# Performance work log

Measured on AMD Instinct MI355X. Metric: run time of the kernel, lower is better.

Reference implementation:

```python
import jax, jax.numpy as jnp
import numpy as np
from jax import lax

K = 3
PAD = 1
K2 = K * K


def _conv(x, w, b):
    dn = lax.conv_dimension_numbers(x.shape, w.shape, ('NCHW', 'OIHW', 'NCHW'))
    y = lax.conv_general_dilated(x, w, (1, 1), [(PAD, PAD), (PAD, PAD)], dimension_numbers=dn)
    return y + b[None, :, None, None]


def _gather(x, iy, ix):
    # x: [B,C,H,W]; iy,ix: [B,K2,H,W] int32 -> [B,C,K2,H,W]
    B, C, H, W = x.shape
    flat = x.reshape(B, C, H * W)
    idx = iy * W + ix  # [B,K2,H,W]
    return jax.vmap(lambda xb, ib: xb[:, ib])(flat, idx)


def _deform_conv2d(x, offset_w, offset_b, mask_w, mask_b, weight):
    B, C, H, W = x.shape
    O = weight.shape[0]
    offset = _conv(x, offset_w, offset_b)            # [B,2*K2,H,W]
    mask = jax.nn.sigmoid(_conv(x, mask_w, mask_b))  # [B,K2,H,W]

    off = offset.reshape(B, K2, 2, H, W)
    oy, ox = off[:, :, 0], off[:, :, 1]              # [B,K2,H,W]

    ki = (jnp.arange(K2) // K).astype(x.dtype)       # kernel row per tap
    kj = (jnp.arange(K2) % K).astype(x.dtype)        # kernel col per tap
    base_y = (jnp.arange(H) - PAD).astype(x.dtype)
    base_x = (jnp.arange(W) - PAD).astype(x.dtype)

    py = oy + base_y[None, None, :, None] + ki[None, :, None, None]  # [B,K2,H,W]
    px = ox + base_x[None, None, None, :] + kj[None, :, None, None]

    y0 = jnp.floor(py)
    x0 = jnp.floor(px)
    dy = py - y0
    dx = px - x0
    y0i = y0.astype(jnp.int32)
    x0i = x0.astype(jnp.int32)

    acc = jnp.zeros((B, C, K2, H, W), dtype=x.dtype)
    for (yc, xc, wgt) in [
        (y0i,     x0i,     (1 - dy) * (1 - dx)),
        (y0i,     x0i + 1, (1 - dy) * dx),
        (y0i + 1, x0i,     dy * (1 - dx)),
        (y0i + 1, x0i + 1, dy * dx),
    ]:
        valid = ((yc >= 0) & (yc < H) & (xc >= 0) & (xc < W)).astype(x.dtype)
        g = _gather(x, jnp.clip(yc, 0, H - 1), jnp.clip(xc, 0, W - 1))  # [B,C,K2,H,W]
        acc = acc + g * (wgt * valid)[:, None]

    modulated = acc * mask[:, None]                  # [B,C,K2,H,W]
    w2 = weight.reshape(O, C, K2)
    return jnp.einsum('bckhw,ock->bohw', modulated, w2)


def setup_inputs() -> dict:
    key = jax.random.key(0)
    ks = jax.random.split(key, 6)
    B, C, O, H, W = 4, 64, 64, 128, 128
    return {
        'x': jax.random.normal(ks[0], (B, C, H, W), jnp.float32),
        'offset_w': jax.random.normal(ks[1], (2 * K2, C, K, K), jnp.float32) * 0.05,
        'offset_b': jax.random.normal(ks[2], (2 * K2,), jnp.float32) * 0.05,
        'mask_w': jax.random.normal(ks[3], (K2, C, K, K), jnp.float32) * 0.05,
        'mask_b': jnp.full((K2,), 0.5, jnp.float32),
        'weight': jax.random.normal(ks[5], (O, C, K, K), jnp.float32) * (1.0 / np.sqrt(C * K2)),
    }


def reference(x, offset_w, offset_b, mask_w, mask_b, weight):
    return _deform_conv2d(x, offset_w, offset_b, mask_w, mask_b, weight)
```

## Files before the change

### kernel.cpp

```cpp
#include <hip/hip_runtime.h>
#include <math.h>

#define BB 4
#define CC 64
#define OO 64
#define HH 128
#define WW 128
#define HWsz (HH * WW)

typedef __attribute__((ext_vector_type(8))) _Float16 half8;
typedef __attribute__((ext_vector_type(4))) float floatx4;

__global__ __launch_bounds__(256) void pre_kernel(
    const float* __restrict__ x, const float* __restrict__ wgt,
    const float* __restrict__ ow, const float* __restrict__ mw,
    _Float16* __restrict__ xh, _Float16* __restrict__ waf,
    _Float16* __restrict__ wcf)
{
    int bid = blockIdx.x;
    int tid = threadIdx.x;
    if (bid < 512) {
        int b = bid >> 7, y = bid & 127;
        int px = tid & 127;
        int ch = (tid >> 7) * 32;
        const float* xp = x + (size_t)(b * CC + ch) * HWsz + y * WW + px;
        _Float16 buf[32];
#pragma unroll
        for (int q = 0; q < 32; ++q)
            buf[q] = (_Float16)xp[(size_t)q * HWsz];
        _Float16* dst = xh + ((size_t)(b * HH + y) * WW + px) * 64 + ch;
#pragma unroll
        for (int q = 0; q < 4; ++q)
            *(half8*)&dst[q * 8] = *(const half8*)&buf[q * 8];
    } else {
        int i = (bid - 512) * 256 + tid;
        if (i < 36864) {
            int j = i & 7, lane = (i >> 3) & 63, rest = i >> 9;
            int m = rest & 3, kh = (rest >> 2) & 1, k = rest >> 3;
            int o = m * 16 + (lane & 15);
            int c = kh * 32 + ((lane >> 4) << 3) + j;
            waf[i] = (_Float16)wgt[o * 576 + c * 9 + k];
        } else if (i < 55296) {
            int t = i - 36864;
            int j = t & 7, lane = (t >> 3) & 63, rest = t >> 9;
            int m = rest & 1, kh = (rest >> 1) & 1, k = rest >> 2;
            int o = m * 16 + (lane & 15);
            int c = kh * 32 + ((lane >> 4) << 3) + j;
            float v = 0.f;
            if (o < 18) v = ow[o * 576 + c * 9 + k];
            else if (o < 27) v = mw[(o - 18) * 576 + c * 9 + k];
            wcf[t] = (_Float16)v;
        }
    }
}

__global__ __launch_bounds__(1024, 1) void fused_kernel(
    const _Float16* __restrict__ wsrc, const _Float16* __restrict__ xh,
    const float* __restrict__ ob, const float* __restrict__ mb,
    float* __restrict__ out)
{
    __shared__ __align__(16) _Float16 lds_w[55296];
    __shared__ _Float16 omh[16 * 27 * 16];
    __shared__ __align__(16) _Float16 bounce[16 * 1152];

    int tid = threadIdx.x;
    int gid = blockIdx.x;
    int sid = (gid & 7) * 32 + (gid >> 3);
    int b = sid >> 6;
    int t = sid & 63;
    int rq = t >> 1;
    int q = t & 1;

    int wv = tid >> 6;
    int lane = tid & 63;
    int s = wv & 3;
    int h = rq * 4 + (wv >> 2);
    int p0 = q << 6;
    int g = lane >> 4;
    int pl = lane & 15;
    int oct = lane & 7;
    int pxg = lane >> 3;

    const _Float16* xhb = xh + ((size_t)b << 20);
    _Float16* omw = &omh[wv * 27 * 16];
    _Float16* bbw = &bounce[wv * 1152];

#pragma unroll
    for (int it = 0; it < 7; ++it) {
        int c = it * 1024 + tid;
        if (c < 6912)
            *(half8*)&lds_w[c * 8] = *(const half8*)(wsrc + c * 8);
    }
    __syncthreads();

    floatx4 accC0 = {0.f, 0.f, 0.f, 0.f};
    floatx4 accC1 = {0.f, 0.f, 0.f, 0.f};

#define STAGE_ROW(KY) do {                                                   \
    int gy = h + (KY) - 1;                                                   \
    half8 z = {0, 0, 0, 0, 0, 0, 0, 0};                                      \
    _Pragma("unroll") for (int j = 0; j < 3; ++j) {                          \
        int pxi = j * 8 + pxg;                                               \
        bool act = (j < 2) | (pxg < 2);                                      \
        int col = p0 + s * 16 - 1 + pxi;                                     \
        bool val = act & (gy >= 0) & (gy < HH) & (col >= 0) & (col < WW);    \
        half8 v = z;                                                         \
        if (val)                                                             \
            v = *(const half8*)(xhb + (((size_t)gy * WW + col) << 6) + oct * 8); \
        if (act)                                                             \
            *(half8*)&bbw[(pxi << 6) + ((oct ^ (pxi & 7)) << 3)] = v;        \
    }                                                                        \
} while (0)

#define CONVT(KY, KX) do {                                                   \
    int K = (KY) * 3 + (KX);                                                 \
    int pc = pl + (KX);                                                      \
    half8 a0 = *(const half8*)&bbw[(pc << 6) + ((g ^ (pc & 7)) << 3)];       \
    half8 a1 = *(const half8*)&bbw[(pc << 6) + (((g + 4) ^ (pc & 7)) << 3)]; \
    const _Float16* wp = &lds_w[36864 + (K << 11) + lane * 8];               \
    half8 w00 = *(const half8*)(wp + (0 << 9));                              \
    half8 w01 = *(const half8*)(wp + (1 << 9));                              \
    half8 w10 = *(const half8*)(wp + (2 << 9));                              \
    half8 w11 = *(const half8*)(wp + (3 << 9));                              \
    accC0 = __builtin_amdgcn_mfma_f32_16x16x32_f16(w00, a0, accC0, 0, 0, 0); \
    accC1 = __builtin_amdgcn_mfma_f32_16x16x32_f16(w01, a0, accC1, 0, 0, 0); \
    accC0 = __builtin_amdgcn_mfma_f32_16x16x32_f16(w10, a1, accC0, 0, 0, 0); \
    accC1 = __builtin_amdgcn_mfma_f32_16x16x32_f16(w11, a1, accC1, 0, 0, 0); \
} while (0)

    STAGE_ROW(0); CONVT(0, 0); CONVT(0, 1); CONVT(0, 2);
    STAGE_ROW(1); CONVT(1, 0); CONVT(1, 1); CONVT(1, 2);
    STAGE_ROW(2); CONVT(2, 0); CONVT(2, 1); CONVT(2, 2);

#pragma unroll
    for (int j = 0; j < 4; ++j) {
        int o = g * 4 + j;
        omw[o * 16 + pl] = (_Float16)(accC0[j] + ob[o]);
        int o2 = 16 + g * 4 + j;
        float v = accC1[j];
        if (o2 < 18) omw[o2 * 16 + pl] = (_Float16)(v + ob[o2]);
        else if (o2 < 27)
            omw[o2 * 16 + pl] =
                (_Float16)(1.0f / (1.0f + expf(-(v + mb[o2 - 18]))));
    }

    floatx4 acc0 = {0.f, 0.f, 0.f, 0.f}, acc1 = {0.f, 0.f, 0.f, 0.f};
    floatx4 acc2 = {0.f, 0.f, 0.f, 0.f}, acc3 = {0.f, 0.f, 0.f, 0.f};

#define MKT(K, P, U00, U01, U10, U11, I00, I01, I10, I11) do {               \
    int ky = (K) / 3, kx = (K) - ky * 3;                                     \
    float oy = (float)omw[(2 * (K)) * 16 + (P)];                             \
    float ox = (float)omw[(2 * (K) + 1) * 16 + (P)];                         \
    float mk = (float)omw[(18 + (K)) * 16 + (P)];                            \
    float py = oy + (float)(h + ky - 1);                                     \
    float qx = ox + (float)(p0 + s * 16 + (P) + kx - 1);                     \
    float y0f = floorf(py), x0f = floorf(qx);                                \
    float dyy = py - y0f, dxx = qx - x0f;                                    \
    int y0 = (int)y0f, x0 = (int)x0f;                                        \
    int y1 = y0 + 1, x1 = x0 + 1;                                            \
    bool vy0 = (y0 >= 0) & (y0 < HH), vy1 = (y1 >= 0) & (y1 < HH);           \
    bool vx0 = (x0 >= 0) & (x0 < WW), vx1 = (x1 >= 0) & (x1 < WW);           \
    U00 = (vy0 & vx0) ? (1.f - dyy) * (1.f - dxx) * mk : 0.f;                \
    U01 = (vy0 & vx1) ? (1.f - dyy) * dxx * mk : 0.f;                        \
    U10 = (vy1 & vx0) ? dyy * (1.f - dxx) * mk : 0.f;                        \
    U11 = (vy1 & vx1) ? dyy * dxx * mk : 0.f;                                \
    int yc0 = min(max(y0, 0), HH - 1), yc1 = min(max(y1, 0), HH - 1);        \
    int xc0 = min(max(x0, 0), WW - 1), xc1 = min(max(x1, 0), WW - 1);        \
    I00 = ((yc0 * WW + xc0) << 6) + oct * 8;                                 \
    I01 = ((yc0 * WW + xc1) << 6) + oct * 8;                                 \
    I10 = ((yc1 * WW + xc0) << 6) + oct * 8;                                 \
    I11 = ((yc1 * WW + xc1) << 6) + oct * 8;                                 \
} while (0)

#define SPLAT8(H) ((half8){(H), (H), (H), (H), (H), (H), (H), (H)})
#define MF(Q, B, A) A = __builtin_amdgcn_mfma_f32_16x16x32_f16(Q, B, A, 0, 0, 0)

#define TAP(K) do {                                                          \
    float uA0, uA1, uA2, uA3, uB0, uB1, uB2, uB3;                            \
    int iA0, iA1, iA2, iA3, iB0, iB1, iB2, iB3;                              \
    MKT(K, pxg, uA0, uA1, uA2, uA3, iA0, iA1, iA2, iA3);                     \
    MKT(K, 8 + pxg, uB0, uB1, uB2, uB3, iB0, iB1, iB2, iB3);                 \
    half8 a0 = *(const half8*)(xhb + iA0);                                   \
    half8 a1 = *(const half8*)(xhb + iA1);                                   \
    half8 a2 = *(const half8*)(xhb + iA2);                                   \
    half8 a3 = *(const half8*)(xhb + iA3);                                   \
    half8 e0 = *(const half8*)(xhb + iB0);                                   \
    half8 e1 = *(const half8*)(xhb + iB1);                                   \
    half8 e2 = *(const half8*)(xhb + iB2);                                   \
    half8 e3 = *(const half8*)(xhb + iB3);                                   \
    half8 bfA = a0 * SPLAT8((_Float16)uA0);                                  \
    bfA = bfA + a1 * SPLAT8((_Float16)uA1);                                  \
    bfA = bfA + a2 * SPLAT8((_Float16)uA2);                                  \
    bfA = bfA + a3 * SPLAT8((_Float16)uA3);                                  \
    half8 bfB = e0 * SPLAT8((_Float16)uB0);                                  \
    bfB = bfB + e1 * SPLAT8((_Float16)uB1);                                  \
    bfB = bfB + e2 * SPLAT8((_Float16)uB2);                                  \
    bfB = bfB + e3 * SPLAT8((_Float16)uB3);                                  \
    *(half8*)&bbw[(pxg << 6) + ((oct ^ pxg) << 3)] = bfA;                    \
    *(half8*)&bbw[((8 + pxg) << 6) + ((oct ^ pxg) << 3)] = bfB;              \
    half8 bf = *(const half8*)&bbw[(pl << 6) + ((g ^ (pl & 7)) << 3)];       \
    half8 bd = *(const half8*)&bbw[(pl << 6) + (((g + 4) ^ (pl & 7)) << 3)]; \
    const _Float16* wk = &lds_w[((K) << 12) + lane * 8];                     \
    half8 q0 = *(const half8*)(wk + (0 << 9));                               \
    half8 q1 = *(const half8*)(wk + (1 << 9));                               \
    half8 q2 = *(const half8*)(wk + (2 << 9));                               \
    half8 q3 = *(const half8*)(wk + (3 << 9));                               \
    half8 q4 = *(const half8*)(wk + (4 << 9));                               \
    half8 q5 = *(const half8*)(wk + (5 << 9));                               \
    half8 q6 = *(const half8*)(wk + (6 << 9));                               \
    half8 q7 = *(const half8*)(wk + (7 << 9));                               \
    MF(q0, bf, acc0); MF(q1, bf, acc1); MF(q2, bf, acc2); MF(q3, bf, acc3);  \
    MF(q4, bd, acc0); MF(q5, bd, acc1); MF(q6, bd, acc2); MF(q7, bd, acc3);  \
} while (0)

    TAP(0); TAP(1); TAP(2); TAP(3); TAP(4); TAP(5); TAP(6); TAP(7); TAP(8);

    float* outp = out + (size_t)b * OO * HWsz + h * WW + p0 + s * 16 + pl;
#pragma unroll
    for (int j = 0; j < 4; ++j) outp[(size_t)(g * 4 + j) * HWsz] = acc0[j];
#pragma unroll
    for (int j = 0; j < 4; ++j) outp[(size_t)(16 + g * 4 + j) * HWsz] = acc1[j];
#pragma unroll
    for (int j = 0; j < 4; ++j) outp[(size_t)(32 + g * 4 + j) * HWsz] = acc2[j];
#pragma unroll
    for (int j = 0; j < 4; ++j) outp[(size_t)(48 + g * 4 + j) * HWsz] = acc3[j];
}

extern "C" void kernel_launch(void* const* d_in, const int* in_sizes, int n_in,
                              void* d_out, int out_size, void* d_ws, size_t ws_size,
                              hipStream_t stream)
{
    const float* x   = (const float*)d_in[0];
    const float* ow  = (const float*)d_in[1];
    const float* ob  = (const float*)d_in[2];
    const float* mw  = (const float*)d_in[3];
    const float* mb  = (const float*)d_in[4];
    const float* wgt = (const float*)d_in[5];
    float* out = (float*)d_out;

    _Float16* xh  = (_Float16*)d_ws;
    _Float16* waf = xh + (size_t)BB * HWsz * 64;
    _Float16* wcf = waf + 36864;

    pre_kernel<<<dim3(512 + 216), dim3(256), 0, stream>>>(
        x, wgt, ow, mw, xh, waf, wcf);
    fused_kernel<<<dim3(256), dim3(1024), 0, stream>>>(
        waf, xh, ob, mb, out);
}
```

Before: 37.43 us.

## Pair deformable taps to issue twice the gathers, with double-buffered LDS bounce

The deformable stage now handles taps in pairs. Each pair issues 16 gather loads before any blend/MFMA, and the two taps use separate LDS bounce buffers. The second buffer reuses the offset-conv weight region, which is dead after the first conv, via one pooled shared array guarded by a new __syncthreads. Offsets are stored interleaved as packed y/x halves and read with one 32-bit LDS load per tap, with the mask kept separately. The aim is to hide global gather latency with more loads in flight, at the cost of higher register pressure with 1024 threads per block.

Result: no change. 37.95 us (+1.4%).

```diff
diff --git a/kernel.cpp b/kernel.cpp
--- a/kernel.cpp
+++ b/kernel.cpp
@@ -10,6 +10,12 @@
 
 typedef __attribute__((ext_vector_type(8))) _Float16 half8;
 typedef __attribute__((ext_vector_type(4))) float floatx4;
+
+static __device__ __forceinline__ float h2f(unsigned u) {
+    union { unsigned short s; _Float16 h; } v;
+    v.s = (unsigned short)u;
+    return (float)v.h;
+}
 
 __global__ __launch_bounds__(256) void pre_kernel(
     const float* __restrict__ x, const float* __restrict__ wgt,
@@ -59,9 +65,7 @@
     const float* __restrict__ ob, const float* __restrict__ mb,
     float* __restrict__ out)
 {
-    __shared__ __align__(16) _Float16 lds_w[55296];
-    __shared__ _Float16 omh[16 * 27 * 16];
-    __shared__ __align__(16) _Float16 bounce[16 * 1152];
+    __shared__ __align__(16) _Float16 pool[80640];
 
     int tid = threadIdx.x;
     int gid = blockIdx.x;
@@ -82,14 +86,16 @@
     int pxg = lane >> 3;
 
     const _Float16* xhb = xh + ((size_t)b << 20);
-    _Float16* omw = &omh[wv * 27 * 16];
-    _Float16* bbw = &bounce[wv * 1152];
+    _Float16* omyx = pool + 55296;
+    _Float16* omm  = pool + 59904;
+    _Float16* bb1  = pool + 62208 + wv * 1152;
+    _Float16* bb2  = pool + 36864 + wv * 1024;
 
 #pragma unroll
     for (int it = 0; it < 7; ++it) {
         int c = it * 1024 + tid;
         if (c < 6912)
-            *(half8*)&lds_w[c * 8] = *(const half8*)(wsrc + c * 8);
+            *(half8*)&pool[c * 8] = *(const half8*)(wsrc + c * 8);
     }
     __syncthreads();
 
@@ -108,16 +114,16 @@
         if (val)                                                             \
             v = *(const half8*)(xhb + (((size_t)gy * WW + col) << 6) + oct * 8); \
         if (act)                                                             \
-            *(half8*)&bbw[(pxi << 6) + ((oct ^ (pxi & 7)) << 3)] = v;        \
+            *(half8*)&bb1[(pxi << 6) + ((oct ^ (pxi & 7)) << 3)] = v;        \
     }                                                                        \
 } while (0)
 
 #define CONVT(KY, KX) do {                                                   \
     int K = (KY) * 3 + (KX);                                                 \
     int pc = pl + (KX);                                                      \
-    half8 a0 = *(const half8*)&bbw[(pc << 6) + ((g ^ (pc & 7)) << 3)];       \
-    half8 a1 = *(const half8*)&bbw[(pc << 6) + (((g + 4) ^ (pc & 7)) << 3)]; \
-    const _Float16* wp = &lds_w[36864 + (K << 11) + lane * 8];               \
+    half8 a0 = *(const half8*)&bb1[(pc << 6) + ((g ^ (pc & 7)) << 3)];       \
+    half8 a1 = *(const half8*)&bb1[(pc << 6) + (((g + 4) ^ (pc & 7)) << 3)]; \
+    const _Float16* wp = &pool[36864 + (K << 11) + lane * 8];                \
     half8 w00 = *(const half8*)(wp + (0 << 9));                              \
     half8 w01 = *(const half8*)(wp + (1 << 9));                              \
     half8 w10 = *(const half8*)(wp + (2 << 9));                              \
@@ -132,28 +138,37 @@
     STAGE_ROW(1); CONVT(1, 0); CONVT(1, 1); CONVT(1, 2);
     STAGE_ROW(2); CONVT(2, 0); CONVT(2, 1); CONVT(2, 2);
 
-#pragma unroll
-    for (int j = 0; j < 4; ++j) {
-        int o = g * 4 + j;
-        omw[o * 16 + pl] = (_Float16)(accC0[j] + ob[o]);
-        int o2 = 16 + g * 4 + j;
-        float v = accC1[j];
-        if (o2 < 18) omw[o2 * 16 + pl] = (_Float16)(v + ob[o2]);
-        else if (o2 < 27)
-            omw[o2 * 16 + pl] =
-                (_Float16)(1.0f / (1.0f + expf(-(v + mb[o2 - 18]))));
+    {
+        int pxbase = ((wv << 4) + pl) * 9;
+#pragma unroll
+        for (int j = 0; j < 4; ++j) {
+            int o = g * 4 + j;
+            omyx[(pxbase + (o >> 1)) * 2 + (o & 1)] = (_Float16)(accC0[j] + ob[o]);
+            int o2 = 16 + g * 4 + j;
+            float v = accC1[j];
+            if (o2 < 18)
+                omyx[(pxbase + (o2 >> 1)) * 2 + (o2 & 1)] = (_Float16)(v + ob[o2]);
+            else if (o2 < 27)
+                omm[pxbase + (o2 - 18)] =
+                    (_Float16)(1.0f / (1.0f + expf(-(v + mb[o2 - 18]))));
+        }
     }
+    __syncthreads();
 
     floatx4 acc0 = {0.f, 0.f, 0.f, 0.f}, acc1 = {0.f, 0.f, 0.f, 0.f};
     floatx4 acc2 = {0.f, 0.f, 0.f, 0.f}, acc3 = {0.f, 0.f, 0.f, 0.f};
 
-#define MKT(K, P, U00, U01, U10, U11, I00, I01, I10, I11) do {               \
+    int pbA = ((wv << 4) + pxg) * 9;
+    int pbB = ((wv << 4) + 8 + pxg) * 9;
+
+#define MKP(K, PB, PX, U00, U01, U10, U11, I00, I01, I10, I11) do {          \
     int ky = (K) / 3, kx = (K) - ky * 3;                                     \
-    float oy = (float)omw[(2 * (K)) * 16 + (P)];                             \
-    float ox = (float)omw[(2 * (K) + 1) * 16 + (P)];                         \
-    float mk = (float)omw[(18 + (K)) * 16 + (P)];                            \
+    unsigned pk_ = *(const unsigned*)&omyx[((PB) + (K)) * 2];                \
+    float oy = h2f(pk_ & 0xffffu);                                           \
+    float ox = h2f(pk_ >> 16);                                               \
+    float mk = (float)omm[(PB) + (K)];                                       \
     float py = oy + (float)(h + ky - 1);                                     \
-    float qx = ox + (float)(p0 + s * 16 + (P) + kx - 1);                     \
+    float qx = ox + (float)(p0 + s * 16 + (PX) + kx - 1);                    \
     float y0f = floorf(py), x0f = floorf(qx);                                \
     float dyy = py - y0f, dxx = qx - x0f;                                    \
     int y0 = (int)y0f, x0 = (int)x0f;                                        \
@@ -175,32 +190,21 @@
 #define SPLAT8(H) ((half8){(H), (H), (H), (H), (H), (H), (H), (H)})
 #define MF(Q, B, A) A = __builtin_amdgcn_mfma_f32_16x16x32_f16(Q, B, A, 0, 0, 0)
 
-#define TAP(K) do {                                                          \
-    float uA0, uA1, uA2, uA3, uB0, uB1, uB2, uB3;                            \
-    int iA0, iA1, iA2, iA3, iB0, iB1, iB2, iB3;                              \
-    MKT(K, pxg, uA0, uA1, uA2, uA3, iA0, iA1, iA2, iA3);                     \
-    MKT(K, 8 + pxg, uB0, uB1, uB2, uB3, iB0, iB1, iB2, iB3);                 \
-    half8 a0 = *(const half8*)(xhb + iA0);                                   \
-    half8 a1 = *(const half8*)(xhb + iA1);                                   \
-    half8 a2 = *(const half8*)(xhb + iA2);                                   \
-    half8 a3 = *(const half8*)(xhb + iA3);                                   \
-    half8 e0 = *(const half8*)(xhb + iB0);                                   \
-    half8 e1 = *(const half8*)(xhb + iB1);                                   \
-    half8 e2 = *(const half8*)(xhb + iB2);                                   \
-    half8 e3 = *(const half8*)(xhb + iB3);                                   \
-    half8 bfA = a0 * SPLAT8((_Float16)uA0);                                  \
-    bfA = bfA + a1 * SPLAT8((_Float16)uA1);                                  \
-    bfA = bfA + a2 * SPLAT8((_Float16)uA2);                                  \
-    bfA = bfA + a3 * SPLAT8((_Float16)uA3);                                  \
-    half8 bfB = e0 * SPLAT8((_Float16)uB0);                                  \
-    bfB = bfB + e1 * SPLAT8((_Float16)uB1);                                  \
-    bfB = bfB + e2 * SPLAT8((_Float16)uB2);                                  \
-    bfB = bfB + e3 * SPLAT8((_Float16)uB3);                                  \
-    *(half8*)&bbw[(pxg << 6) + ((oct ^ pxg) << 3)] = bfA;                    \
-    *(half8*)&bbw[((8 + pxg) << 6) + ((oct ^ pxg) << 3)] = bfB;              \
-    half8 bf = *(const half8*)&bbw[(pl << 6) + ((g ^ (pl & 7)) << 3)];       \
-    half8 bd = *(const half8*)&bbw[(pl << 6) + (((g + 4) ^ (pl & 7)) << 3)]; \
-    const _Float16* wk = &lds_w[((K) << 12) + lane * 8];                     \
+#define PROC(K, BB, A0, A1, A2, A3, E0, E1, E2, E3,                          \
+             U0, U1, U2, U3, V0, V1, V2, V3) do {                            \
+    half8 bfA = A0 * SPLAT8((_Float16)U0);                                   \
+    bfA = bfA + A1 * SPLAT8((_Float16)U1);                                   \
+    bfA = bfA + A2 * SPLAT8((_Float16)U2);                                   \
+    bfA = bfA + A3 * SPLAT8((_Float16)U3);                                   \
+    half8 bfB = E0 * SPLAT8((_Float16)V0);                                   \
+    bfB = bfB + E1 * SPLAT8((_Float16)V1);                                   \
+    bfB = bfB + E2 * SPLAT8((_Float16)V2);                                   \
+    bfB = bfB + E3 * SPLAT8((_Float16)V3);                                   \
+    *(half8*)&(BB)[(pxg << 6) + ((oct ^ pxg) << 3)] = bfA;                   \
+    *(half8*)&(BB)[((8 + pxg) << 6) + ((oct ^ pxg) << 3)] = bfB;             \
+    half8 bf = *(const half8*)&(BB)[(pl << 6) + ((g ^ (pl & 7)) << 3)];      \
+    half8 bd = *(const half8*)&(BB)[(pl << 6) + (((g + 4) ^ (pl & 7)) << 3)];\
+    const _Float16* wk = &pool[((K) << 12) + lane * 8];                      \
     half8 q0 = *(const half8*)(wk + (0 << 9));                               \
     half8 q1 = *(const half8*)(wk + (1 << 9));                               \
     half8 q2 = *(const half8*)(wk + (2 << 9));                               \
@@ -213,7 +217,59 @@
     MF(q4, bd, acc0); MF(q5, bd, acc1); MF(q6, bd, acc2); MF(q7, bd, acc3);  \
 } while (0)
 
-    TAP(0); TAP(1); TAP(2); TAP(3); TAP(4); TAP(5); TAP(6); TAP(7); TAP(8);
+#define TAPPAIR(K) do {                                                      \
+    float uA0, uA1, uA2, uA3, uB0, uB1, uB2, uB3;                            \
+    float uC0, uC1, uC2, uC3, uD0, uD1, uD2, uD3;                            \
+    int iA0, iA1, iA2, iA3, iB0, iB1, iB2, iB3;                              \
+    int iC0, iC1, iC2, iC3, iD0, iD1, iD2, iD3;                              \
+    MKP(K, pbA, pxg, uA0, uA1, uA2, uA3, iA0, iA1, iA2, iA3);                \
+    MKP(K, pbB, 8 + pxg, uB0, uB1, uB2, uB3, iB0, iB1, iB2, iB3);            \
+    MKP((K) + 1, pbA, pxg, uC0, uC1, uC2, uC3, iC0, iC1, iC2, iC3);          \
+    MKP((K) + 1, pbB, 8 + pxg, uD0, uD1, uD2, uD3, iD0, iD1, iD2, iD3);      \
+    half8 a0 = *(const half8*)(xhb + iA0);                                   \
+    half8 a1 = *(const half8*)(xhb + iA1);                                   \
+    half8 a2 = *(const half8*)(xhb + iA2);                                   \
+    half8 a3 = *(const half8*)(xhb + iA3);                                   \
+    half8 e0 = *(const half8*)(xhb + iB0);                                   \
+    half8 e1 = *(const half8*)(xhb + iB1);                                   \
+    half8 e2 = *(const half8*)(xhb + iB2);                                   \
+    half8 e3 = *(const half8*)(xhb + iB3);                                   \
+    half8 c0 = *(const half8*)(xhb + iC0);                                   \
+    half8 c1 = *(const half8*)(xhb + iC1);                                   \
+    half8 c2 = *(const half8*)(xhb + iC2);                                   \
+    half8 c3 = *(const half8*)(xhb + iC3);                                   \
+    half8 f0 = *(const half8*)(xhb + iD0);                                   \
+    half8 f1 = *(const half8*)(xhb + iD1);                                   \
+    half8 f2 = *(const half8*)(xhb + iD2);                                   \
+    half8 f3 = *(const half8*)(xhb + iD3);                                   \
+    PROC(K, bb1, a0, a1, a2, a3, e0, e1, e2, e3,                             \
+         uA0, uA1, uA2, uA3, uB0, uB1, uB2, uB3);                            \
+    PROC((K) + 1, bb2, c0, c1, c2, c3, f0, f1, f2, f3,                       \
+         uC0, uC1, uC2, uC3, uD0, uD1, uD2, uD3);                            \
+} while (0)
+
+#define TAPSOLO(K) do {                                                      \
+    float uA0, uA1, uA2, uA3, uB0, uB1, uB2, uB3;                            \
+    int iA0, iA1, iA2, iA3, iB0, iB1, iB2, iB3;                              \
+    MKP(K, pbA, pxg, uA0, uA1, uA2, uA3, iA0, iA1, iA2, iA3);                \
+    MKP(K, pbB, 8 + pxg, uB0, uB1, uB2, uB3, iB0, iB1, iB2, iB3);            \
+    half8 a0 = *(const half8*)(xhb + iA0);                                   \
+    half8 a1 = *(const half8*)(xhb + iA1);                                   \
+    half8 a2 = *(const half8*)(xhb + iA2);                                   \
+    half8 a3 = *(const half8*)(xhb + iA3);                                   \
+    half8 e0 = *(const half8*)(xhb + iB0);                                   \
+    half8 e1 = *(const half8*)(xhb + iB1);                                   \
+    half8 e2 = *(const half8*)(xhb + iB2);                                   \
+    half8 e3 = *(const half8*)(xhb + iB3);                                   \
+    PROC(K, bb1, a0, a1, a2, a3, e0, e1, e2, e3,                             \
+         uA0, uA1, uA2, uA3, uB0, uB1, uB2, uB3);                            \
+} while (0)
+
+    TAPPAIR(0);
+    TAPPAIR(2);
+    TAPPAIR(4);
+    TAPPAIR(6);
+    TAPSOLO(8);
 
     float* outp = out + (size_t)b * OO * HWsz + h * WW + p0 + s * 16 + pl;
 #pragma unroll
```
